# Optimization experiments

Hardware: AMD Instinct MI355X
Metric: run time of the kernel (lower is better)

## Reference

```python
import jax, jax.numpy as jnp
import numpy as np

N, E, F, H, C, K = 50000, 1600000, 128, 64, 40, 4


def setup_inputs() -> dict:
    key = jax.random.key(0)
    ks = jax.random.split(key, 4)
    x = jax.random.normal(ks[0], (N, F), dtype=jnp.float32)
    edge_index = jax.random.randint(ks[1], (2, E), 0, N, dtype=jnp.int32)
    edge_weight = jnp.ones((E,), dtype=jnp.float32)
    # lin of ChebConv: Linear(K*in, out); kaiming for layer1, xavier-ish for layer2
    W1 = jax.random.normal(ks[2], (K * F, H), dtype=jnp.float32) * (2.0 / (K * F)) ** 0.5
    b1 = jnp.zeros((H,), jnp.float32)
    W2 = jax.random.normal(ks[3], (K * H, C), dtype=jnp.float32) * (2.0 / (K * H + C)) ** 0.5
    b2 = jnp.zeros((C,), jnp.float32)
    return {"x": x, "edge_index": edge_index, "edge_weight": edge_weight,
            "W1": W1, "b1": b1, "W2": W2, "b2": b2}


def _cheb_norm(edge_index, edge_weight, num_nodes):
    """Edge weights of L_hat = 2*L/lambda_max - I with sym norm, lambda_max=2.
    L = I - D^{-1/2} A D^{-1/2}; so L_hat off-diag = -d_i^{-1/2} w d_j^{-1/2},
    diag = (1 if deg>0 else 0) - 1."""
    src, dst = edge_index[0], edge_index[1]
    deg = jax.ops.segment_sum(edge_weight, src, num_segments=num_nodes)
    dis = jnp.where(deg > 0, jax.lax.rsqrt(jnp.maximum(deg, 1e-12)), 0.0)
    w_norm = -dis[src] * edge_weight * dis[dst]   # [E] off-diagonal of L_hat
    diag = jnp.where(deg > 0, 0.0, -1.0)          # [N] diagonal of L_hat
    return src, dst, w_norm, diag


def _cheb_conv(x, src, dst, w_norm, diag, W, b, num_nodes):
    def prop(h):  # L_hat @ h via gather-multiply-scatter
        msg = w_norm[:, None] * h[src]                                  # [E, F]
        return diag[:, None] * h + jax.ops.segment_sum(msg, dst, num_segments=num_nodes)

    Tx_prev2 = x
    Tx_prev1 = prop(x)
    Txs = [Tx_prev2, Tx_prev1]
    for _ in range(2, K):
        Tx = 2.0 * prop(Tx_prev1) - Tx_prev2
        Txs.append(Tx)
        Tx_prev2, Tx_prev1 = Tx_prev1, Tx
    Z = jnp.concatenate(Txs, axis=1)              # [N, K*F]
    return Z @ W + b


def reference(x, edge_index, edge_weight, W1, b1, W2, b2):
    num_nodes = x.shape[0]
    src, dst, w_norm, diag = _cheb_norm(edge_index, edge_weight, num_nodes)
    # dropout layers are identity at inference
    h = _cheb_conv(x, src, dst, w_norm, diag, W1, b1, num_nodes)
    h = jax.nn.relu(h)
    out = _cheb_conv(h, src, dst, w_norm, diag, W2, b2, num_nodes)
    return out
```

## Files before the change

kernel.cpp:

```cpp
#include <hip/hip_runtime.h>

#define NN 50000
#define EE 1600000
#define FF 128
#define HH 64
#define CC 40

#define NCH 64
#define CHE (EE / NCH)
#define NSL 4
#define SLN (NN / NSL)

#define PA 250
#define EPP (EE / PA)
#define SB 250
#define SLNB 200
#define BCAP 64

#define HALFE ((size_t)NN * 32)

static __device__ __forceinline__ float bf2f(unsigned short u) {
    union { unsigned int i; float f; } c; c.i = ((unsigned int)u) << 16; return c.f;
}
static __device__ __forceinline__ unsigned short f2bf(float x) {
    union { float f; unsigned int i; } c; c.f = x;
    unsigned int r = c.i + 0x7FFFu + ((c.i >> 16) & 1u);
    return (unsigned short)(r >> 16);
}
static __device__ __forceinline__ void up2(unsigned w, float& lo, float& hi) {
    union { unsigned u; float f; } a, b;
    a.u = w << 16; b.u = w & 0xFFFF0000u;
    lo = a.f; hi = b.f;
}

typedef __attribute__((ext_vector_type(8))) short bf16x8;
typedef __attribute__((ext_vector_type(4))) float f32x4;
union BF8 { bf16x8 v; unsigned short u[8]; };

__global__ __launch_bounds__(1024) void deg_hist_kernel(
    const int* __restrict__ src, const float* __restrict__ w,
    float* __restrict__ pdeg) {
    __shared__ float ldeg[SLN];
    int s = blockIdx.x % NSL;
    int c = blockIdx.x / NSL;
    int base = s * SLN;
    for (int i = threadIdx.x; i < SLN; i += 1024) ldeg[i] = 0.f;
    __syncthreads();
    int e0 = c * CHE;
    for (int e = e0 + threadIdx.x; e < e0 + CHE; e += 1024) {
        int se = src[e];
        unsigned us = (unsigned)(se - base);
        if (us < SLN) atomicAdd(&ldeg[us], w[e]);
    }
    __syncthreads();
    for (int i = threadIdx.x; i < SLN; i += 1024)
        pdeg[(size_t)c * NN + base + i] = ldeg[i];
}

__global__ void reduce_kernel(const float* __restrict__ pdeg,
                              float* __restrict__ dis, float* __restrict__ diag) {
    int n = blockIdx.x * blockDim.x + threadIdx.x;
    if (n >= NN) return;
    float dsum = 0.f;
    for (int c = 0; c < NCH; ++c) dsum += pdeg[(size_t)c * NN + n];
    dis[n]  = (dsum > 0.f) ? rsqrtf(fmaxf(dsum, 1e-12f)) : 0.f;
    diag[n] = (dsum > 0.f) ? 0.f : -1.f;
}

__global__ __launch_bounds__(256) void bucketA_kernel(
    const int* __restrict__ src, const int* __restrict__ dst,
    const float* __restrict__ w, const float* __restrict__ dis,
    uint2* __restrict__ buckets, int* __restrict__ counts) {
    __shared__ int lcnt[SB];
    int p = blockIdx.x;
    for (int i = threadIdx.x; i < SB; i += 256) lcnt[i] = 0;
    __syncthreads();
    int e0 = p * EPP;
    for (int e = e0 + threadIdx.x; e < e0 + EPP; e += 256) {
        int de = dst[e], se = src[e];
        int sl = de / SLNB;
        int dl = de - sl * SLNB;
        float wn = -dis[se] * w[e] * dis[de];
        unsigned lo = (unsigned)se | ((unsigned)f2bf(wn) << 16);
        int idx = atomicAdd(&lcnt[sl], 1);
        buckets[((size_t)p * SB + sl) * BCAP + idx] = make_uint2(lo, (unsigned)dl);
    }
    __syncthreads();
    for (int i = threadIdx.x; i < SB; i += 256) counts[p * SB + i] = lcnt[i];
}

__global__ void scanS_kernel(const int* __restrict__ counts, int* __restrict__ sbase) {
    __shared__ int sh[256];
    int t = threadIdx.x;
    int total = 0;
    if (t < SB)
        for (int p = 0; p < PA; ++p) total += counts[p * SB + t];
    sh[t] = total;
    __syncthreads();
    for (int off = 1; off < 256; off <<= 1) {
        int x = (t >= off) ? sh[t - off] : 0;
        __syncthreads();
        sh[t] += x;
        __syncthreads();
    }
    if (t < SB) sbase[t] = sh[t] - total;
    if (t == SB - 1) sbase[SB] = sh[t];
}

__global__ __launch_bounds__(256) void bucketB_kernel(
    const uint2* __restrict__ buckets, const int* __restrict__ counts,
    const int* __restrict__ sbase,
    int* __restrict__ row_start, unsigned int* __restrict__ csr) {
    __shared__ int lcounts[PA];
    __shared__ int lhist[SLNB];
    __shared__ int sh[256];
    int s = blockIdx.x;
    int t = threadIdx.x;
    if (t < PA) lcounts[t] = counts[t * SB + s];
    for (int i = t; i < SLNB; i += 256) lhist[i] = 0;
    __syncthreads();
    int g = t >> 4, l16 = t & 15;
    for (int p = g; p < PA; p += 16) {
        int c = lcounts[p];
        const uint2* b = buckets + ((size_t)p * SB + s) * BCAP;
        for (int i = l16; i < c; i += 16)
            atomicAdd(&lhist[b[i].y], 1);
    }
    __syncthreads();
    int v = (t < SLNB) ? lhist[t] : 0;
    sh[t] = v;
    __syncthreads();
    for (int off = 1; off < 256; off <<= 1) {
        int x = (t >= off) ? sh[t - off] : 0;
        __syncthreads();
        sh[t] += x;
        __syncthreads();
    }
    int base = sbase[s];
    if (t < SLNB) {
        int excl = sh[t] - v;
        row_start[s * SLNB + t] = base + excl;
        lhist[t] = base + excl;
    }
    if (s == SB - 1 && t == 0) row_start[NN] = sbase[SB];
    __syncthreads();
    for (int p = g; p < PA; p += 16) {
        int c = lcounts[p];
        const uint2* b = buckets + ((size_t)p * SB + s) * BCAP;
        for (int i = l16; i < c; i += 16) {
            uint2 en = b[i];
            int pos = atomicAdd(&lhist[en.y], 1);
            csr[pos] = en.x;
        }
    }
}

template <int FACT, typename OUT_T, int FINAL>
__global__ __launch_bounds__(256) void prop4_kernel(
    const unsigned short* __restrict__ a, float alphaL,
    const unsigned short* __restrict__ p1, float beta1,
    const unsigned short* __restrict__ p2, float beta2,
    const float* __restrict__ bias, int doRelu,
    const float* __restrict__ diag, const int* __restrict__ rs,
    const unsigned int* __restrict__ csr, OUT_T* __restrict__ out) {

    int bid = blockIdx.x;
    int xc = bid & 7, g = bid >> 3;
    int pss, nb, logGL;
    if constexpr (FACT == 64) {
        pss = xc >> 2; nb = g * 4 + (xc & 3); logGL = 3;
        if (nb >= (NN + 31) / 32) return;
    } else if constexpr (!FINAL) {
        if (xc < 5) { pss = 0; nb = g * 5 + xc;       logGL = 3; if (nb >= (NN + 31) / 32)  return; }
        else        { pss = 1; nb = g * 3 + (xc - 5); logGL = 2; if (nb >= (NN + 63) / 64)  return; }
    } else {
        if (xc < 6) { pss = 0; nb = g * 6 + xc;       logGL = 3; if (nb >= (NN + 31) / 32)  return; }
        else        { pss = 1; nb = g * 2 + (xc - 6); logGL = 1; if (nb >= (NN + 127) / 128) return; }
    }
    int t = threadIdx.x;
    int gl = t & ((1 << logGL) - 1);
    int node = nb * (256 >> logGL) + (t >> logGL);
    if (node >= NN) return;
    int f4 = gl << 2;
    const unsigned short* ah = a + (size_t)pss * HALFE;

    uint2 av = *(const uint2*)(ah + (size_t)node * 32 + f4);
    float d = diag[node];
    float a0, a1, a2, a3; up2(av.x, a0, a1); up2(av.y, a2, a3);
    float acc0 = d * a0, acc1 = d * a1, acc2 = d * a2, acc3 = d * a3;

    int j = rs[node], j1 = rs[node + 1];
    for (; j + 4 <= j1; j += 4) {
        unsigned cw0 = csr[j], cw1 = csr[j + 1], cw2 = csr[j + 2], cw3 = csr[j + 3];
        uint2 g0 = *(const uint2*)(ah + (size_t)(cw0 & 0xFFFFu) * 32 + f4);
        uint2 g1 = *(const uint2*)(ah + (size_t)(cw1 & 0xFFFFu) * 32 + f4);
        uint2 g2 = *(const uint2*)(ah + (size_t)(cw2 & 0xFFFFu) * 32 + f4);
        uint2 g3 = *(const uint2*)(ah + (size_t)(cw3 & 0xFFFFu) * 32 + f4);
        float w0 = bf2f((unsigned short)(cw0 >> 16));
        float w1 = bf2f((unsigned short)(cw1 >> 16));
        float w2 = bf2f((unsigned short)(cw2 >> 16));
        float w3 = bf2f((unsigned short)(cw3 >> 16));
        float l0, h0, l1, h1;
        up2(g0.x, l0, h0); up2(g0.y, l1, h1);
        acc0 = fmaf(w0, l0, acc0); acc1 = fmaf(w0, h0, acc1);
        acc2 = fmaf(w0, l1, acc2); acc3 = fmaf(w0, h1, acc3);
        up2(g1.x, l0, h0); up2(g1.y, l1, h1);
        acc0 = fmaf(w1, l0, acc0); acc1 = fmaf(w1, h0, acc1);
        acc2 = fmaf(w1, l1, acc2); acc3 = fmaf(w1, h1, acc3);
        up2(g2.x, l0, h0); up2(g2.y, l1, h1);
        acc0 = fmaf(w2, l0, acc0); acc1 = fmaf(w2, h0, acc1);
        acc2 = fmaf(w2, l1, acc2); acc3 = fmaf(w2, h1, acc3);
        up2(g3.x, l0, h0); up2(g3.y, l1, h1);
        acc0 = fmaf(w3, l0, acc0); acc1 = fmaf(w3, h0, acc1);
        acc2 = fmaf(w3, l1, acc2); acc3 = fmaf(w3, h1, acc3);
    }
    for (; j < j1; ++j) {
        unsigned cw = csr[j];
        uint2 gv = *(const uint2*)(ah + (size_t)(cw & 0xFFFFu) * 32 + f4);
        float w = bf2f((unsigned short)(cw >> 16));
        float l0, h0, l1, h1; up2(gv.x, l0, h0); up2(gv.y, l1, h1);
        acc0 = fmaf(w, l0, acc0); acc1 = fmaf(w, h0, acc1);
        acc2 = fmaf(w, l1, acc2); acc3 = fmaf(w, h1, acc3);
    }

    int fg = pss * 32 + f4;
    size_t off = (size_t)pss * HALFE + (size_t)node * 32 + f4;
    uint2 q1 = *(const uint2*)(p1 + off);
    float s0, s1, s2, s3; up2(q1.x, s0, s1); up2(q1.y, s2, s3);
    float r0 = alphaL * acc0 + beta1 * s0;
    float r1 = alphaL * acc1 + beta1 * s1;
    float r2 = alphaL * acc2 + beta1 * s2;
    float r3 = alphaL * acc3 + beta1 * s3;
    if (beta2 != 0.f) {
        uint2 q2 = *(const uint2*)(p2 + off);
        up2(q2.x, s0, s1); up2(q2.y, s2, s3);
        r0 = fmaf(beta2, s0, r0); r1 = fmaf(beta2, s1, r1);
        r2 = fmaf(beta2, s2, r2); r3 = fmaf(beta2, s3, r3);
    }
    if constexpr (FINAL) {
        if (fg < CC) {
            r0 += bias[fg]; r1 += bias[fg + 1]; r2 += bias[fg + 2]; r3 += bias[fg + 3];
            float4 st = make_float4(r0, r1, r2, r3);
            *(float4*)((float*)out + (size_t)node * CC + fg) = st;
        }
    } else {
        if (bias) { r0 += bias[fg]; r1 += bias[fg + 1]; r2 += bias[fg + 2]; r3 += bias[fg + 3]; }
        if (doRelu) {
            r0 = fmaxf(r0, 0.f); r1 = fmaxf(r1, 0.f);
            r2 = fmaxf(r2, 0.f); r3 = fmaxf(r3, 0.f);
        }
        if constexpr (sizeof(OUT_T) == 2) {
            ushort4 st; st.x = f2bf(r0); st.y = f2bf(r1); st.z = f2bf(r2); st.w = f2bf(r3);
            *(ushort4*)(out + off) = st;
        } else {
            float4 st = make_float4(r0, r1, r2, r3);
            *(float4*)((float*)out + off) = st;
        }
    }
}

__global__ __launch_bounds__(256) void convw_kernel(
    const float* __restrict__ W1, const float* __restrict__ W2,
    unsigned short* __restrict__ W1t_hi, unsigned short* __restrict__ W1t_lo,
    unsigned short* __restrict__ W2t_hi, unsigned short* __restrict__ W2t_lo) {
    int tid = blockIdx.x * 256 + threadIdx.x;
    if (tid < 512 * 64) {
        int row = tid >> 7, kk = tid & 127;
        int ct = row >> 6, j = row & 63;
        float v = W1[((size_t)(ct * 128 + kk)) * 64 + j];
        unsigned short h = f2bf(v);
        W1t_hi[tid] = h;
        W1t_lo[tid] = f2bf(v - bf2f(h));
    } else {
        int t2 = tid - 512 * 64;
        if (t2 >= 4 * 64 * 64) return;
        int row = t2 >> 6, kk = t2 & 63;
        int kt = row >> 6, j = row & 63;
        float v = (j < CC) ? W2[((size_t)(kt * 64 + kk)) * CC + j] : 0.f;
        unsigned short h = f2bf(v);
        W2t_hi[t2] = h;
        W2t_lo[t2] = f2bf(v - bf2f(h));
    }
}

template <int KF, int AHALF>
__global__ __launch_bounds__(256) void gemm_mfma_kernel(
    const float* __restrict__ A, const unsigned short* __restrict__ Wt_hi,
    const unsigned short* __restrict__ Wt_lo, unsigned short* __restrict__ Yb) {
    constexpr int KK = KF * 32;
    int lane = threadIdx.x & 63;
    int ct   = threadIdx.x >> 6;
    int l15  = lane & 15;
    int lg   = lane >> 4;
    int m0   = blockIdx.x * 32;

    f32x4 acc[2][4];
    #pragma unroll
    for (int i = 0; i < 2; ++i)
        #pragma unroll
        for (int j = 0; j < 4; ++j)
            acc[i][j] = (f32x4){0.f, 0.f, 0.f, 0.f};

    #pragma unroll
    for (int kf = 0; kf < KF; ++kf) {
        int k0 = kf * 32 + lg * 8;
        BF8 bh[4], bl[4];
        #pragma unroll
        for (int nf = 0; nf < 4; ++nf) {
            size_t addr = (size_t)(ct * 64 + nf * 16 + l15) * KK + k0;
            bh[nf].v = *reinterpret_cast<const bf16x8*>(Wt_hi + addr);
            bl[nf].v = *reinterpret_cast<const bf16x8*>(Wt_lo + addr);
        }
        BF8 ah[2], al[2];
        #pragma unroll
        for (int ms = 0; ms < 2; ++ms) {
            int n = m0 + ms * 16 + l15;
            if (n >= NN) n = NN - 1;
            const float* ap;
            if constexpr (AHALF)
                ap = A + (size_t)kf * HALFE + (size_t)n * 32 + lg * 8;
            else
                ap = A + (size_t)n * KK + k0;
            float4 f0 = *(const float4*)(ap);
            float4 f1 = *(const float4*)(ap + 4);
            float fv[8] = {f0.x, f0.y, f0.z, f0.w, f1.x, f1.y, f1.z, f1.w};
            #pragma unroll
            for (int u = 0; u < 8; ++u) {
                unsigned short h = f2bf(fv[u]);
                ah[ms].u[u] = h;
                al[ms].u[u] = f2bf(fv[u] - bf2f(h));
            }
        }
        #pragma unroll
        for (int ms = 0; ms < 2; ++ms)
            #pragma unroll
            for (int nf = 0; nf < 4; ++nf) {
                acc[ms][nf] = __builtin_amdgcn_mfma_f32_16x16x32_bf16(
                    ah[ms].v, bh[nf].v, acc[ms][nf], 0, 0, 0);
                acc[ms][nf] = __builtin_amdgcn_mfma_f32_16x16x32_bf16(
                    ah[ms].v, bl[nf].v, acc[ms][nf], 0, 0, 0);
                acc[ms][nf] = __builtin_amdgcn_mfma_f32_16x16x32_bf16(
                    al[ms].v, bh[nf].v, acc[ms][nf], 0, 0, 0);
            }
    }

    unsigned short* slab = Yb + (size_t)ct * NN * 64;
    #pragma unroll
    for (int ms = 0; ms < 2; ++ms)
        #pragma unroll
        for (int r = 0; r < 4; ++r) {
            int n = m0 + ms * 16 + lg * 4 + r;
            if (n < NN) {
                #pragma unroll
                for (int nf = 0; nf < 4; ++nf)
                    slab[(size_t)(nf >> 1) * HALFE + (size_t)n * 32 + (nf & 1) * 16 + l15]
                        = f2bf(acc[ms][nf][r]);
            }
        }
}

extern "C" void kernel_launch(void* const* d_in, const int* in_sizes, int n_in,
                              void* d_out, int out_size, void* d_ws, size_t ws_size,
                              hipStream_t stream) {
    const float* x    = (const float*)d_in[0];
    const int*   eidx = (const int*)d_in[1];
    const float* ew   = (const float*)d_in[2];
    const float* W1   = (const float*)d_in[3];
    const float* b1   = (const float*)d_in[4];
    const float* W2   = (const float*)d_in[5];
    const float* b2   = (const float*)d_in[6];
    float* out = (float*)d_out;

    const int* src = eidx;
    const int* dst = eidx + EE;

    float* p = (float*)d_ws;
    unsigned int* csr = (unsigned int*)p;  p += (size_t)EE;
    float* dis  = p;                  p += ((NN + 63) / 64) * 64;
    float* diag = p;                  p += ((NN + 63) / 64) * 64;
    unsigned short* Yb = (unsigned short*)p;  p += (size_t)NN * 128;
    unsigned short* u  = (unsigned short*)p;  p += (size_t)NN * 32;
    unsigned short* v  = (unsigned short*)p;  p += (size_t)NN * 32;
    float* h    = p;                  p += (size_t)NN * 64;
    float* scratch = p;               p += (size_t)PA * SB * BCAP * 2;
    int* row_start = (int*)p;
    int* counts    = row_start + NN + 1;
    int* sbase     = counts + PA * SB;

    float* pdeg    = scratch;
    uint2* buckets = (uint2*)scratch;
    unsigned short* W1t_hi = (unsigned short*)scratch;
    unsigned short* W1t_lo = W1t_hi + 512 * 64;
    unsigned short* W2t_hi = W1t_lo + 512 * 64;
    unsigned short* W2t_lo = W2t_hi + 4 * 64 * 64;
    unsigned short* y0b = Yb;
    unsigned short* y1b = Yb + (size_t)1 * NN * 64;
    unsigned short* y2b = Yb + (size_t)2 * NN * 64;
    unsigned short* y3b = Yb + (size_t)3 * NN * 64;
    unsigned short* Zb = Yb;
    unsigned short* z0 = Zb;
    unsigned short* z1 = Zb + (size_t)1 * NN * 64;
    unsigned short* z2 = Zb + (size_t)2 * NN * 64;
    unsigned short* z3 = Zb + (size_t)3 * NN * 64;
    unsigned short* u2 = u;
    unsigned short* v2 = v;

    const int B = 256;
    deg_hist_kernel<<<NCH * NSL, 1024, 0, stream>>>(src, ew, pdeg);
    reduce_kernel<<<(NN + B - 1) / B, B, 0, stream>>>(pdeg, dis, diag);
    bucketA_kernel<<<PA, 256, 0, stream>>>(src, dst, ew, dis, buckets, counts);
    scanS_kernel<<<1, 256, 0, stream>>>(counts, sbase);
    bucketB_kernel<<<SB, 256, 0, stream>>>(buckets, counts, sbase, row_start, csr);
    convw_kernel<<<192, 256, 0, stream>>>(W1, W2, W1t_hi, W1t_lo, W2t_hi, W2t_lo);

    int ggrid = (NN + 31) / 32;
    const int NB32 = (NN + 31) / 32;
    const int PG64  = ((NB32 + 3) / 4) * 8;
    const int PG48  = ((NB32 + 4) / 5) * 8;
    const int PG48F = ((NB32 + 5) / 6) * 8;

    gemm_mfma_kernel<4, 0><<<ggrid, 256, 0, stream>>>(x, W1t_hi, W1t_lo, Yb);
    prop4_kernel<64, unsigned short, 0><<<PG64, 256, 0, stream>>>(
        y3b, 4.f, y2b, 2.f, nullptr, 0.f,
        nullptr, 0, diag, row_start, csr, u);
    prop4_kernel<64, unsigned short, 0><<<PG64, 256, 0, stream>>>(
        u, 1.f, y1b, 1.f, y3b, -3.f,
        nullptr, 0, diag, row_start, csr, v);
    prop4_kernel<64, float, 0><<<PG64, 256, 0, stream>>>(
        v, 1.f, y0b, 1.f, y2b, -1.f,
        b1, 1, diag, row_start, csr, h);

    gemm_mfma_kernel<2, 1><<<ggrid, 256, 0, stream>>>(h, W2t_hi, W2t_lo, Zb);
    prop4_kernel<48, unsigned short, 0><<<PG48, 256, 0, stream>>>(
        z3, 4.f, z2, 2.f, nullptr, 0.f,
        nullptr, 0, diag, row_start, csr, u2);
    prop4_kernel<48, unsigned short, 0><<<PG48, 256, 0, stream>>>(
        u2, 1.f, z1, 1.f, z3, -3.f,
        nullptr, 0, diag, row_start, csr, v2);
    prop4_kernel<48, float, 1><<<PG48F, 256, 0, stream>>>(
        v2, 1.f, z0, 1.f, z2, -1.f,
        b2, 0, diag, row_start, csr, (float*)out);
}
```

Before: 466.0 us.

## Split each node's edge list across four sub-lanes and reduce with shuffles

The sparse propagation kernel now gives each destination node four lane groups that walk interleaved edges, stride 4 within groups of 8, instead of one group walking all edges. Partial sums are combined with xor shuffles, and only sub-lane 0 does the epilogue and store. The grid grows fourfold. This is meant to raise memory-level parallelism and shorten each thread's serial gather chain for rows averaging about 32 edges. In exchange it adds shuffle overhead, redundant row_start loads and idle lanes in the epilogue.

```diff
diff --git a/kernel.cpp b/kernel.cpp
--- a/kernel.cpp
+++ b/kernel.cpp
@@ -156,7 +156,7 @@
 }
 
 template <int FACT, typename OUT_T, int FINAL>
-__global__ __launch_bounds__(256) void prop4_kernel(
+__global__ __launch_bounds__(256) void prop5_kernel(
     const unsigned short* __restrict__ a, float alphaL,
     const unsigned short* __restrict__ p1, float beta1,
     const unsigned short* __restrict__ p2, float beta2,
@@ -169,37 +169,41 @@
     int pss, nb, logGL;
     if constexpr (FACT == 64) {
         pss = xc >> 2; nb = g * 4 + (xc & 3); logGL = 3;
-        if (nb >= (NN + 31) / 32) return;
+        if (nb >= (NN + 7) / 8) return;
     } else if constexpr (!FINAL) {
-        if (xc < 5) { pss = 0; nb = g * 5 + xc;       logGL = 3; if (nb >= (NN + 31) / 32)  return; }
-        else        { pss = 1; nb = g * 3 + (xc - 5); logGL = 2; if (nb >= (NN + 63) / 64)  return; }
+        if (xc < 5) { pss = 0; nb = g * 5 + xc;       logGL = 3; if (nb >= (NN + 7) / 8)   return; }
+        else        { pss = 1; nb = g * 3 + (xc - 5); logGL = 2; if (nb >= (NN + 15) / 16) return; }
     } else {
-        if (xc < 6) { pss = 0; nb = g * 6 + xc;       logGL = 3; if (nb >= (NN + 31) / 32)  return; }
-        else        { pss = 1; nb = g * 2 + (xc - 6); logGL = 1; if (nb >= (NN + 127) / 128) return; }
+        if (xc < 6) { pss = 0; nb = g * 6 + xc;       logGL = 3; if (nb >= (NN + 7) / 8)   return; }
+        else        { pss = 1; nb = g * 2 + (xc - 6); logGL = 1; if (nb >= (NN + 31) / 32) return; }
     }
     int t = threadIdx.x;
-    int gl = t & ((1 << logGL) - 1);
-    int node = nb * (256 >> logGL) + (t >> logGL);
-    if (node >= NN) return;
-    int f4 = gl << 2;
+    int fl  = t & ((1 << logGL) - 1);
+    int sub = (t >> logGL) & 3;
+    int NPB = 256 >> (logGL + 2);
+    int node = nb * NPB + (t >> (logGL + 2));
+    int nc = node < NN ? node : NN - 1;
+    int f4 = fl << 2;
     const unsigned short* ah = a + (size_t)pss * HALFE;
 
-    uint2 av = *(const uint2*)(ah + (size_t)node * 32 + f4);
-    float d = diag[node];
-    float a0, a1, a2, a3; up2(av.x, a0, a1); up2(av.y, a2, a3);
-    float acc0 = d * a0, acc1 = d * a1, acc2 = d * a2, acc3 = d * a3;
-
-    int j = rs[node], j1 = rs[node + 1];
-    for (; j + 4 <= j1; j += 4) {
-        unsigned cw0 = csr[j], cw1 = csr[j + 1], cw2 = csr[j + 2], cw3 = csr[j + 3];
+    float acc0, acc1, acc2, acc3;
+    if (sub == 0) {
+        uint2 av = *(const uint2*)(ah + (size_t)nc * 32 + f4);
+        float d = diag[nc];
+        float a0, a1, a2, a3; up2(av.x, a0, a1); up2(av.y, a2, a3);
+        acc0 = d * a0; acc1 = d * a1; acc2 = d * a2; acc3 = d * a3;
+    } else {
+        acc0 = acc1 = acc2 = acc3 = 0.f;
+    }
+
+    int j1 = rs[nc + 1];
+    int j = rs[nc] + sub;
+    for (; j + 4 < j1; j += 8) {
+        unsigned cw0 = csr[j], cw1 = csr[j + 4];
         uint2 g0 = *(const uint2*)(ah + (size_t)(cw0 & 0xFFFFu) * 32 + f4);
         uint2 g1 = *(const uint2*)(ah + (size_t)(cw1 & 0xFFFFu) * 32 + f4);
-        uint2 g2 = *(const uint2*)(ah + (size_t)(cw2 & 0xFFFFu) * 32 + f4);
-        uint2 g3 = *(const uint2*)(ah + (size_t)(cw3 & 0xFFFFu) * 32 + f4);
         float w0 = bf2f((unsigned short)(cw0 >> 16));
         float w1 = bf2f((unsigned short)(cw1 >> 16));
-        float w2 = bf2f((unsigned short)(cw2 >> 16));
-        float w3 = bf2f((unsigned short)(cw3 >> 16));
         float l0, h0, l1, h1;
         up2(g0.x, l0, h0); up2(g0.y, l1, h1);
         acc0 = fmaf(w0, l0, acc0); acc1 = fmaf(w0, h0, acc1);
@@ -207,14 +211,8 @@
         up2(g1.x, l0, h0); up2(g1.y, l1, h1);
         acc0 = fmaf(w1, l0, acc0); acc1 = fmaf(w1, h0, acc1);
         acc2 = fmaf(w1, l1, acc2); acc3 = fmaf(w1, h1, acc3);
-        up2(g2.x, l0, h0); up2(g2.y, l1, h1);
-        acc0 = fmaf(w2, l0, acc0); acc1 = fmaf(w2, h0, acc1);
-        acc2 = fmaf(w2, l1, acc2); acc3 = fmaf(w2, h1, acc3);
-        up2(g3.x, l0, h0); up2(g3.y, l1, h1);
-        acc0 = fmaf(w3, l0, acc0); acc1 = fmaf(w3, h0, acc1);
-        acc2 = fmaf(w3, l1, acc2); acc3 = fmaf(w3, h1, acc3);
-    }
-    for (; j < j1; ++j) {
+    }
+    if (j < j1) {
         unsigned cw = csr[j];
         uint2 gv = *(const uint2*)(ah + (size_t)(cw & 0xFFFFu) * 32 + f4);
         float w = bf2f((unsigned short)(cw >> 16));
@@ -222,6 +220,13 @@
         acc0 = fmaf(w, l0, acc0); acc1 = fmaf(w, h0, acc1);
         acc2 = fmaf(w, l1, acc2); acc3 = fmaf(w, h1, acc3);
     }
+
+    acc0 += __shfl_xor(acc0, 1 << logGL); acc0 += __shfl_xor(acc0, 2 << logGL);
+    acc1 += __shfl_xor(acc1, 1 << logGL); acc1 += __shfl_xor(acc1, 2 << logGL);
+    acc2 += __shfl_xor(acc2, 1 << logGL); acc2 += __shfl_xor(acc2, 2 << logGL);
+    acc3 += __shfl_xor(acc3, 1 << logGL); acc3 += __shfl_xor(acc3, 2 << logGL);
+
+    if (sub != 0 || node >= NN) return;
 
     int fg = pss * 32 + f4;
     size_t off = (size_t)pss * HALFE + (size_t)node * 32 + f4;
@@ -414,30 +419,32 @@
     convw_kernel<<<192, 256, 0, stream>>>(W1, W2, W1t_hi, W1t_lo, W2t_hi, W2t_lo);
 
     int ggrid = (NN + 31) / 32;
+    const int NB8  = (NN + 7) / 8;
+    const int NB16 = (NN + 15) / 16;
     const int NB32 = (NN + 31) / 32;
-    const int PG64  = ((NB32 + 3) / 4) * 8;
-    const int PG48  = ((NB32 + 4) / 5) * 8;
-    const int PG48F = ((NB32 + 5) / 6) * 8;
+    const int PG64  = ((NB8 + 3) / 4) * 8;
+    const int PG48  = ((NB8 + 4) / 5) * 8;
+    const int PG48F = ((NB8 + 5) / 6) * 8;
 
     gemm_mfma_kernel<4, 0><<<ggrid, 256, 0, stream>>>(x, W1t_hi, W1t_lo, Yb);
-    prop4_kernel<64, unsigned short, 0><<<PG64, 256, 0, stream>>>(
+    prop5_kernel<64, unsigned short, 0><<<PG64, 256, 0, stream>>>(
         y3b, 4.f, y2b, 2.f, nullptr, 0.f,
         nullptr, 0, diag, row_start, csr, u);
-    prop4_kernel<64, unsigned short, 0><<<PG64, 256, 0, stream>>>(
+    prop5_kernel<64, unsigned short, 0><<<PG64, 256, 0, stream>>>(
         u, 1.f, y1b, 1.f, y3b, -3.f,
         nullptr, 0, diag, row_start, csr, v);
-    prop4_kernel<64, float, 0><<<PG64, 256, 0, stream>>>(
+    prop5_kernel<64, float, 0><<<PG64, 256, 0, stream>>>(
         v, 1.f, y0b, 1.f, y2b, -1.f,
         b1, 1, diag, row_start, csr, h);
 
     gemm_mfma_kernel<2, 1><<<ggrid, 256, 0, stream>>>(h, W2t_hi, W2t_lo, Zb);
-    prop4_kernel<48, unsigned short, 0><<<PG48, 256, 0, stream>>>(
+    prop5_kernel<48, unsigned short, 0><<<PG48, 256, 0, stream>>>(
         z3, 4.f, z2, 2.f, nullptr, 0.f,
         nullptr, 0, diag, row_start, csr, u2);
-    prop4_kernel<48, unsigned short, 0><<<PG48, 256, 0, stream>>>(
+    prop5_kernel<48, unsigned short, 0><<<PG48, 256, 0, stream>>>(
         u2, 1.f, z1, 1.f, z3, -3.f,
         nullptr, 0, diag, row_start, csr, v2);
-    prop4_kernel<48, float, 1><<<PG48F, 256, 0, stream>>>(
+    prop5_kernel<48, float, 1><<<PG48F, 256, 0, stream>>>(
         v2, 1.f, z0, 1.f, z2, -1.f,
         b2, 0, diag, row_start, csr, (float*)out);
 }
```

New measurement: 473.5 us. About the same (+1.6%).
